# Performance work log

Hardware: AMD Instinct MI355X
Metric: run time of the kernel (lower is better)

Reference implementation:

```python
import jax, jax.numpy as jnp
import numpy as np

B, T, C, H = 256, 256, 384, 64  # batch, seq (= block_size), n_embd, head_size


def setup_inputs() -> dict:
    key = jax.random.key(0)
    kx, kq, kk, kv = jax.random.split(key, 4)
    x = jax.random.normal(kx, (B, T, C), dtype=jnp.float32)
    # nn.Linear(n_embd, head_size, bias=False) weights, stored transposed so y = x @ W
    scale = 1.0 / np.sqrt(C)
    Wq = jax.random.normal(kq, (C, H), dtype=jnp.float32) * scale
    Wk = jax.random.normal(kk, (C, H), dtype=jnp.float32) * scale
    Wv = jax.random.normal(kv, (C, H), dtype=jnp.float32) * scale
    return {"x": x, "Wq": Wq, "Wk": Wk, "Wv": Wv}


def reference(x, Wq, Wk, Wv):
    # Single causal self-attention head. NOTE: source scales by C**-0.5 where
    # C = n_embd (not head_size) — preserved faithfully. Dropout in eval mode
    # (identity) for a deterministic reference.
    Bv, Tv, Cv = x.shape
    q = x @ Wq                                   # [B, T, H]
    k = x @ Wk                                   # [B, T, H]
    v = x @ Wv                                   # [B, T, H]
    wei = jnp.einsum('bth,bsh->bts', q, k) * (Cv ** -0.5)  # [B, T, T]
    causal = jnp.tril(jnp.ones((Tv, Tv), dtype=bool))      # tril[:T,:T]
    wei = jnp.where(causal[None, :, :], wei, -jnp.inf)
    wei = jax.nn.softmax(wei, axis=-1)
    out = jnp.einsum('bts,bsh->bth', wei, v)     # [B, T, H]
    return out
```

## Files before the change

kernel.cpp:

```cpp
#include <hip/hip_runtime.h>
#include <hip/hip_bf16.h>

typedef __attribute__((ext_vector_type(8))) short bf16x8;
typedef __attribute__((ext_vector_type(4))) float f32x4;

__device__ __forceinline__ unsigned short f2bf(float f) {
    union { float f; unsigned int u; } v; v.f = f;
    unsigned int u = v.u;
    unsigned int r = u + 0x7FFFu + ((u >> 16) & 1u);
    return (unsigned short)(r >> 16);
}

#define GLDS16(gsrc, ldst)                                                          \
    __builtin_amdgcn_global_load_lds(                                               \
        (const __attribute__((address_space(1))) unsigned int*)(gsrc),              \
        (__attribute__((address_space(3))) unsigned int*)(ldst), 16, 0, 0)

__global__ __launch_bounds__(256) void wprep(const float* __restrict__ Wq,
                                             const float* __restrict__ Wk,
                                             const float* __restrict__ Wv,
                                             unsigned short* __restrict__ Wt2) {
    int idx = blockIdx.x * 256 + threadIdx.x;
    if (idx >= 73728) return;
    int w   = idx / 24576;
    int rem = idx % 24576;
    int n = rem / 384, k = rem % 384;
    const float* W = (w == 0) ? Wq : ((w == 1) ? Wk : Wv);
    int col = w * 64 + n;
    Wt2[(size_t)(k >> 5) * 6144 + ((k >> 3) & 3) * 1536 + col * 8 + (k & 7)] = f2bf(W[k * 64 + n]);
}

#define XB0   0
#define XB1   32768
#define BB0   65536
#define BB1   77824
#define QOFF  0
#define KOFF  36864
#define VTOFF 73728
#define POFF  107520

__global__ __launch_bounds__(512, 2) void fused(const float* __restrict__ x,
                                                const unsigned short* __restrict__ Wt2,
                                                float* __restrict__ out) {
    __shared__ __align__(16) char smem[144384];

    const int b = blockIdx.x;
    const int tid = threadIdx.x, lane = tid & 63, wid = tid >> 6;
    const int l15 = lane & 15, lg = lane >> 4;
    const int wr = wid >> 1, wc = wid & 1;
    const float* xb = x + (size_t)b * 98304;
    float* ob = out + (size_t)b * 16384;
    const int xrow8 = lane >> 3;
    const int xphys = lane & 7;

    auto issue = [&](int c) {
        char* xd = smem + ((c & 1) ? XB1 : XB0);
        char* bd = smem + ((c & 1) ? BB1 : BB0);
#pragma unroll
        for (int g = 0; g < 4; ++g) {
            int gg = wid * 4 + g;
            int row = gg * 8 + xrow8;
            int lchunk = xphys ^ (row & 7);
            GLDS16(xb + (size_t)row * 384 + c * 32 + lchunk * 4, xd + gg * 1024);
        }
        if (wid < 4) {
            GLDS16(Wt2 + (size_t)c * 6144 + (wid * 2) * 512 + lane * 8, bd + (wid * 2) * 1024);
            GLDS16(Wt2 + (size_t)c * 6144 + (wid * 2 + 1) * 512 + lane * 8, bd + (wid * 2 + 1) * 1024);
        } else {
            GLDS16(Wt2 + (size_t)c * 6144 + (4 + wid) * 512 + lane * 8, bd + (4 + wid) * 1024);
        }
    };

    f32x4 acc[4][6] = {};
    issue(0);
    issue(1);
#pragma unroll
    for (int c = 0; c < 12; ++c) {
        if (c < 11) {
            if (wid < 4) { asm volatile("s_waitcnt vmcnt(6)" ::: "memory"); }
            else         { asm volatile("s_waitcnt vmcnt(5)" ::: "memory"); }
        } else {
            asm volatile("s_waitcnt vmcnt(0)" ::: "memory");
        }
        __builtin_amdgcn_s_barrier();

        const char* xs = smem + ((c & 1) ? XB1 : XB0);
        const char* bs = smem + ((c & 1) ? BB1 : BB0);
        bf16x8 bfr[6];
#pragma unroll
        for (int n = 0; n < 6; ++n)
            bfr[n] = *reinterpret_cast<const bf16x8*>(bs + lg * 3072 + (wc * 96 + n * 16 + l15) * 16);
        bf16x8 afr[4];
#pragma unroll
        for (int m = 0; m < 4; ++m) {
            int r = wr * 64 + m * 16 + l15;
            int s0 = (2 * lg) ^ (r & 7), s1 = (2 * lg + 1) ^ (r & 7);
            float4 f0 = *reinterpret_cast<const float4*>(xs + r * 128 + s0 * 16);
            float4 f1 = *reinterpret_cast<const float4*>(xs + r * 128 + s1 * 16);
            afr[m][0] = (short)f2bf(f0.x); afr[m][1] = (short)f2bf(f0.y);
            afr[m][2] = (short)f2bf(f0.z); afr[m][3] = (short)f2bf(f0.w);
            afr[m][4] = (short)f2bf(f1.x); afr[m][5] = (short)f2bf(f1.y);
            afr[m][6] = (short)f2bf(f1.z); afr[m][7] = (short)f2bf(f1.w);
        }
#pragma unroll
        for (int m = 0; m < 4; ++m)
#pragma unroll
            for (int n = 0; n < 6; ++n)
                acc[m][n] = __builtin_amdgcn_mfma_f32_16x16x32_bf16(afr[m], bfr[n], acc[m][n], 0, 0, 0);

        __builtin_amdgcn_s_barrier();
        if (c < 10) issue(c + 2);
    }
    __syncthreads();

#pragma unroll
    for (int m = 0; m < 4; ++m) {
#pragma unroll
        for (int n = 0; n < 6; ++n) {
            int colb = wc * 96 + n * 16 + l15;
#pragma unroll
            for (int j = 0; j < 4; ++j) {
                int t = wr * 64 + m * 16 + lg * 4 + j;
                unsigned short hv = f2bf(acc[m][n][j]);
                if (colb < 64)
                    *reinterpret_cast<unsigned short*>(smem + QOFF + (t * 72 + colb) * 2) = hv;
                else if (colb < 128)
                    *reinterpret_cast<unsigned short*>(smem + KOFF + (t * 72 + (colb - 64)) * 2) = hv;
                else
                    *reinterpret_cast<unsigned short*>(smem + VTOFF + ((colb - 128) * 264 + t) * 2) = hv;
            }
        }
    }
    __syncthreads();

    char* Pw = smem + POFF + wid * 4608;
    const int r0 = wid * 32;
    const float scale = 0.05103103630798287f;

    f32x4 o[2][4] = {};
    float M[2][4], L[2][4];
#pragma unroll
    for (int m = 0; m < 2; ++m)
#pragma unroll
        for (int j = 0; j < 4; ++j) { M[m][j] = -1e30f; L[m][j] = 0.f; }

    for (int jt = 0; jt <= (wid >> 1); ++jt) {
        f32x4 s[2][4] = {};
#pragma unroll
        for (int kk = 0; kk < 2; ++kk) {
            bf16x8 aq[2], bk[4];
#pragma unroll
            for (int m = 0; m < 2; ++m)
                aq[m] = *reinterpret_cast<const bf16x8*>(smem + QOFF + ((r0 + m * 16 + l15) * 72 + kk * 32 + lg * 8) * 2);
#pragma unroll
            for (int n = 0; n < 4; ++n)
                bk[n] = *reinterpret_cast<const bf16x8*>(smem + KOFF + ((jt * 64 + n * 16 + l15) * 72 + kk * 32 + lg * 8) * 2);
#pragma unroll
            for (int m = 0; m < 2; ++m)
#pragma unroll
                for (int n = 0; n < 4; ++n)
                    s[m][n] = __builtin_amdgcn_mfma_f32_16x16x32_bf16(aq[m], bk[n], s[m][n], 0, 0, 0);
        }
        float tm[2][4];
#pragma unroll
        for (int m = 0; m < 2; ++m)
#pragma unroll
            for (int j = 0; j < 4; ++j) tm[m][j] = -1e30f;
#pragma unroll
        for (int m = 0; m < 2; ++m) {
#pragma unroll
            for (int n = 0; n < 4; ++n) {
                int colg = jt * 64 + n * 16 + l15;
#pragma unroll
                for (int j = 0; j < 4; ++j) {
                    int rowg = r0 + m * 16 + lg * 4 + j;
                    float v = s[m][n][j] * scale;
                    if (colg > rowg) v = -1e30f;
                    s[m][n][j] = v;
                    tm[m][j] = fmaxf(tm[m][j], v);
                }
            }
        }
#pragma unroll
        for (int m = 0; m < 2; ++m)
#pragma unroll
            for (int j = 0; j < 4; ++j) {
                float v = tm[m][j];
                v = fmaxf(v, __shfl_xor(v, 1));
                v = fmaxf(v, __shfl_xor(v, 2));
                v = fmaxf(v, __shfl_xor(v, 4));
                v = fmaxf(v, __shfl_xor(v, 8));
                tm[m][j] = v;
            }
        float alpha[2][4];
#pragma unroll
        for (int m = 0; m < 2; ++m)
#pragma unroll
            for (int j = 0; j < 4; ++j) {
                float mn = fmaxf(M[m][j], tm[m][j]);
                alpha[m][j] = __expf(M[m][j] - mn);
                M[m][j] = mn;
            }
        float ts[2][4] = {};
#pragma unroll
        for (int m = 0; m < 2; ++m)
#pragma unroll
            for (int n = 0; n < 4; ++n)
#pragma unroll
                for (int j = 0; j < 4; ++j) {
                    float p = __expf(s[m][n][j] - M[m][j]);
                    s[m][n][j] = p;
                    ts[m][j] += p;
                }
#pragma unroll
        for (int m = 0; m < 2; ++m)
#pragma unroll
            for (int j = 0; j < 4; ++j) {
                float v = ts[m][j];
                v += __shfl_xor(v, 1);
                v += __shfl_xor(v, 2);
                v += __shfl_xor(v, 4);
                v += __shfl_xor(v, 8);
                L[m][j] = L[m][j] * alpha[m][j] + v;
            }
#pragma unroll
        for (int m = 0; m < 2; ++m)
#pragma unroll
            for (int n = 0; n < 4; ++n)
#pragma unroll
                for (int j = 0; j < 4; ++j) o[m][n][j] *= alpha[m][j];
#pragma unroll
        for (int m = 0; m < 2; ++m)
#pragma unroll
            for (int n = 0; n < 4; ++n)
#pragma unroll
                for (int j = 0; j < 4; ++j)
                    *reinterpret_cast<unsigned short*>(Pw + ((m * 16 + lg * 4 + j) * 72 + n * 16 + l15) * 2) = f2bf(s[m][n][j]);
        asm volatile("s_waitcnt lgkmcnt(0)" ::: "memory");
#pragma unroll
        for (int kk = 0; kk < 2; ++kk) {
            bf16x8 ap[2], bv[4];
#pragma unroll
            for (int m = 0; m < 2; ++m)
                ap[m] = *reinterpret_cast<const bf16x8*>(Pw + ((m * 16 + l15) * 72 + kk * 32 + lg * 8) * 2);
#pragma unroll
            for (int n = 0; n < 4; ++n)
                bv[n] = *reinterpret_cast<const bf16x8*>(smem + VTOFF + ((n * 16 + l15) * 264 + jt * 64 + kk * 32 + lg * 8) * 2);
#pragma unroll
            for (int m = 0; m < 2; ++m)
#pragma unroll
                for (int n = 0; n < 4; ++n)
                    o[m][n] = __builtin_amdgcn_mfma_f32_16x16x32_bf16(ap[m], bv[n], o[m][n], 0, 0, 0);
        }
    }
#pragma unroll
    for (int m = 0; m < 2; ++m) {
#pragma unroll
        for (int n = 0; n < 4; ++n) {
            int h = n * 16 + l15;
#pragma unroll
            for (int j = 0; j < 4; ++j) {
                int t = r0 + m * 16 + lg * 4 + j;
                ob[(size_t)t * 64 + h] = o[m][n][j] / L[m][j];
            }
        }
    }
}

extern "C" void kernel_launch(void* const* d_in, const int* in_sizes, int n_in,
                              void* d_out, int out_size, void* d_ws, size_t ws_size,
                              hipStream_t stream) {
    const float* x  = (const float*)d_in[0];
    const float* Wq = (const float*)d_in[1];
    const float* Wk = (const float*)d_in[2];
    const float* Wv = (const float*)d_in[3];
    float* out = (float*)d_out;

    unsigned short* Wt2 = (unsigned short*)d_ws;

    wprep<<<288, 256, 0, stream>>>(Wq, Wk, Wv, Wt2);
    fused<<<256, 512, 0, stream>>>(x, Wt2, out);
}
```

Measured before the change: 45.15 us.

## Load full weight matrix to LDS once and stream x directly into registers

The QKV projection stage now loads the whole packed bf16 weight matrix (144 KB) into LDS up front instead of double-buffering it per K-chunk. Each wave now reads its 32 rows of x straight from global memory into registers through a three-deep software pipeline, so x no longer passes through LDS. The fp32-to-bf16 conversion uses the packed v_cvt_pk_bf16_f32 instruction in place of manual rounding. Per-chunk block barriers are removed and each wave owns full rows (2x12 MFMA tiles). The cost is a larger LDS footprint (147456 bytes, which with launch_bounds(512,2) limits how many blocks fit per CU) and more registers for the in-flight x loads.

```diff
diff --git a/kernel.cpp b/kernel.cpp
--- a/kernel.cpp
+++ b/kernel.cpp
@@ -9,6 +9,12 @@
     unsigned int u = v.u;
     unsigned int r = u + 0x7FFFu + ((u >> 16) & 1u);
     return (unsigned short)(r >> 16);
+}
+
+__device__ __forceinline__ unsigned int cvtpk(float lo, float hi) {
+    unsigned int r;
+    asm("v_cvt_pk_bf16_f32 %0, %1, %2" : "=v"(r) : "v"(lo), "v"(hi));
+    return r;
 }
 
 #define GLDS16(gsrc, ldst)                                                          \
@@ -30,10 +36,6 @@
     Wt2[(size_t)(k >> 5) * 6144 + ((k >> 3) & 3) * 1536 + col * 8 + (k & 7)] = f2bf(W[k * 64 + n]);
 }
 
-#define XB0   0
-#define XB1   32768
-#define BB0   65536
-#define BB1   77824
 #define QOFF  0
 #define KOFF  36864
 #define VTOFF 73728
@@ -42,92 +44,88 @@
 __global__ __launch_bounds__(512, 2) void fused(const float* __restrict__ x,
                                                 const unsigned short* __restrict__ Wt2,
                                                 float* __restrict__ out) {
-    __shared__ __align__(16) char smem[144384];
+    __shared__ __align__(16) char smem[147456];
 
     const int b = blockIdx.x;
     const int tid = threadIdx.x, lane = tid & 63, wid = tid >> 6;
     const int l15 = lane & 15, lg = lane >> 4;
-    const int wr = wid >> 1, wc = wid & 1;
     const float* xb = x + (size_t)b * 98304;
     float* ob = out + (size_t)b * 16384;
-    const int xrow8 = lane >> 3;
-    const int xphys = lane & 7;
-
-    auto issue = [&](int c) {
-        char* xd = smem + ((c & 1) ? XB1 : XB0);
-        char* bd = smem + ((c & 1) ? BB1 : BB0);
-#pragma unroll
-        for (int g = 0; g < 4; ++g) {
-            int gg = wid * 4 + g;
-            int row = gg * 8 + xrow8;
-            int lchunk = xphys ^ (row & 7);
-            GLDS16(xb + (size_t)row * 384 + c * 32 + lchunk * 4, xd + gg * 1024);
-        }
-        if (wid < 4) {
-            GLDS16(Wt2 + (size_t)c * 6144 + (wid * 2) * 512 + lane * 8, bd + (wid * 2) * 1024);
-            GLDS16(Wt2 + (size_t)c * 6144 + (wid * 2 + 1) * 512 + lane * 8, bd + (wid * 2 + 1) * 1024);
-        } else {
-            GLDS16(Wt2 + (size_t)c * 6144 + (4 + wid) * 512 + lane * 8, bd + (4 + wid) * 1024);
-        }
-    };
-
-    f32x4 acc[4][6] = {};
-    issue(0);
-    issue(1);
-#pragma unroll
-    for (int c = 0; c < 12; ++c) {
-        if (c < 11) {
-            if (wid < 4) { asm volatile("s_waitcnt vmcnt(6)" ::: "memory"); }
-            else         { asm volatile("s_waitcnt vmcnt(5)" ::: "memory"); }
-        } else {
-            asm volatile("s_waitcnt vmcnt(0)" ::: "memory");
-        }
-        __builtin_amdgcn_s_barrier();
-
-        const char* xs = smem + ((c & 1) ? XB1 : XB0);
-        const char* bs = smem + ((c & 1) ? BB1 : BB0);
-        bf16x8 bfr[6];
-#pragma unroll
-        for (int n = 0; n < 6; ++n)
-            bfr[n] = *reinterpret_cast<const bf16x8*>(bs + lg * 3072 + (wc * 96 + n * 16 + l15) * 16);
-        bf16x8 afr[4];
-#pragma unroll
-        for (int m = 0; m < 4; ++m) {
-            int r = wr * 64 + m * 16 + l15;
-            int s0 = (2 * lg) ^ (r & 7), s1 = (2 * lg + 1) ^ (r & 7);
-            float4 f0 = *reinterpret_cast<const float4*>(xs + r * 128 + s0 * 16);
-            float4 f1 = *reinterpret_cast<const float4*>(xs + r * 128 + s1 * 16);
-            afr[m][0] = (short)f2bf(f0.x); afr[m][1] = (short)f2bf(f0.y);
-            afr[m][2] = (short)f2bf(f0.z); afr[m][3] = (short)f2bf(f0.w);
-            afr[m][4] = (short)f2bf(f1.x); afr[m][5] = (short)f2bf(f1.y);
-            afr[m][6] = (short)f2bf(f1.z); afr[m][7] = (short)f2bf(f1.w);
-        }
-#pragma unroll
-        for (int m = 0; m < 4; ++m)
-#pragma unroll
-            for (int n = 0; n < 6; ++n)
-                acc[m][n] = __builtin_amdgcn_mfma_f32_16x16x32_bf16(afr[m], bfr[n], acc[m][n], 0, 0, 0);
-
-        __builtin_amdgcn_s_barrier();
-        if (c < 10) issue(c + 2);
-    }
+
+#pragma unroll
+    for (int i = 0; i < 18; ++i) {
+        int n = wid * 18 + i;
+        GLDS16(Wt2 + (size_t)n * 512 + lane * 8, smem + n * 1024);
+    }
+
+    const float* xw = xb + (size_t)(wid * 32 + l15) * 384 + lg * 8;
+
+    float4 p0[4], p1[4], p2[4];
+#define XLOAD(P, C)                                                                 \
+    P[0] = *reinterpret_cast<const float4*>(xw + (C) * 32);                         \
+    P[1] = *reinterpret_cast<const float4*>(xw + (C) * 32 + 4);                     \
+    P[2] = *reinterpret_cast<const float4*>(xw + 6144 + (C) * 32);                  \
+    P[3] = *reinterpret_cast<const float4*>(xw + 6144 + (C) * 32 + 4);
+    XLOAD(p0, 0)
+    XLOAD(p1, 1)
+    XLOAD(p2, 2)
+    __builtin_amdgcn_sched_barrier(0);
+    asm volatile("s_waitcnt vmcnt(12)" ::: "memory");
+    __builtin_amdgcn_s_barrier();
+
+    f32x4 acc[2][12] = {};
+
+#define CHUNK(C, P, WAITN)                                                          \
+    asm volatile("s_waitcnt vmcnt(" #WAITN ")" ::: "memory");                       \
+    __builtin_amdgcn_sched_barrier(0);                                              \
+    {                                                                               \
+        union { unsigned int u[4]; bf16x8 v; } cv0, cv1;                            \
+        cv0.u[0] = cvtpk(P[0].x, P[0].y); cv0.u[1] = cvtpk(P[0].z, P[0].w);         \
+        cv0.u[2] = cvtpk(P[1].x, P[1].y); cv0.u[3] = cvtpk(P[1].z, P[1].w);         \
+        cv1.u[0] = cvtpk(P[2].x, P[2].y); cv1.u[1] = cvtpk(P[2].z, P[2].w);         \
+        cv1.u[2] = cvtpk(P[3].x, P[3].y); cv1.u[3] = cvtpk(P[3].z, P[3].w);         \
+        bf16x8 a0 = cv0.v, a1 = cv1.v;                                              \
+        if ((C) + 3 < 12) { XLOAD(P, (C) + 3) }                                     \
+        __builtin_amdgcn_sched_barrier(0);                                          \
+        const char* bs = smem + (C) * 12288 + lg * 3072 + l15 * 16;                 \
+        _Pragma("unroll")                                                           \
+        for (int n = 0; n < 12; ++n) {                                              \
+            bf16x8 bf = *reinterpret_cast<const bf16x8*>(bs + n * 256);             \
+            acc[0][n] = __builtin_amdgcn_mfma_f32_16x16x32_bf16(a0, bf, acc[0][n], 0, 0, 0); \
+            acc[1][n] = __builtin_amdgcn_mfma_f32_16x16x32_bf16(a1, bf, acc[1][n], 0, 0, 0); \
+        }                                                                           \
+    }
+
+    CHUNK(0,  p0, 8)
+    CHUNK(1,  p1, 8)
+    CHUNK(2,  p2, 8)
+    CHUNK(3,  p0, 8)
+    CHUNK(4,  p1, 8)
+    CHUNK(5,  p2, 8)
+    CHUNK(6,  p0, 8)
+    CHUNK(7,  p1, 8)
+    CHUNK(8,  p2, 8)
+    CHUNK(9,  p0, 8)
+    CHUNK(10, p1, 4)
+    CHUNK(11, p2, 0)
+
     __syncthreads();
 
 #pragma unroll
-    for (int m = 0; m < 4; ++m) {
-#pragma unroll
-        for (int n = 0; n < 6; ++n) {
-            int colb = wc * 96 + n * 16 + l15;
-#pragma unroll
-            for (int j = 0; j < 4; ++j) {
-                int t = wr * 64 + m * 16 + lg * 4 + j;
+    for (int m = 0; m < 2; ++m) {
+#pragma unroll
+        for (int n = 0; n < 12; ++n) {
+            int col = n * 16 + l15;
+#pragma unroll
+            for (int j = 0; j < 4; ++j) {
+                int t = wid * 32 + m * 16 + lg * 4 + j;
                 unsigned short hv = f2bf(acc[m][n][j]);
-                if (colb < 64)
-                    *reinterpret_cast<unsigned short*>(smem + QOFF + (t * 72 + colb) * 2) = hv;
-                else if (colb < 128)
-                    *reinterpret_cast<unsigned short*>(smem + KOFF + (t * 72 + (colb - 64)) * 2) = hv;
+                if (col < 64)
+                    *reinterpret_cast<unsigned short*>(smem + QOFF + (t * 72 + col) * 2) = hv;
+                else if (col < 128)
+                    *reinterpret_cast<unsigned short*>(smem + KOFF + (t * 72 + (col - 64)) * 2) = hv;
                 else
-                    *reinterpret_cast<unsigned short*>(smem + VTOFF + ((colb - 128) * 264 + t) * 2) = hv;
+                    *reinterpret_cast<unsigned short*>(smem + VTOFF + ((col - 128) * 264 + t) * 2) = hv;
             }
         }
     }
```

After: 41.09 us. 9.0% less time.
